# Kernel optimization log

Hardware: AMD Instinct MI355X
Metric: run time of the kernel (lower is better)

The kernel has to match this reference:

```python
import jax, jax.numpy as jnp
import numpy as np

EPS = 1e-5      # numerical floor for degrees / std / attenuation
LEAK = 0.01     # LeakyReLU slope of mixing FCLayer
AVG_D = 3.3     # log(avg_degree + 1) from init_kwargs
BIG = 1e30      # masking constant for max/min aggregators


def setup_inputs() -> dict:
    key = jax.random.key(0)
    ks = jax.random.split(key, 12)
    B, N, Din, De, H = 8, 256, 128, 64, 128
    s = 0.05
    inp = {
        "input": jax.random.normal(ks[0], (B, N, Din), jnp.float32),
        "adj": (jax.random.uniform(ks[1], (B, N, N)) < 0.1).astype(jnp.float32),
        "adj_features": jax.random.normal(ks[2], (B, N, N, De), jnp.float32),
        "hidden": jnp.zeros((B * N, H), jnp.float32),
        "pre_W": jax.random.normal(ks[3], (2 * Din + De, Din), jnp.float32) * s,
        "pre_b": jnp.zeros((Din,), jnp.float32),
        "post_W": jax.random.normal(ks[4], (13 * Din, H), jnp.float32) * s,
        "post_b": jnp.zeros((H,), jnp.float32),
        "mix_W": jax.random.normal(ks[5], (H, H), jnp.float32) * s,
        "mix_b": jnp.zeros((H,), jnp.float32),
        "gru_Wih": jax.random.normal(ks[6], (3 * H, H), jnp.float32) * s,
        "gru_Whh": jax.random.normal(ks[7], (3 * H, H), jnp.float32) * s,
    }
    return inp


def reference(input, adj, adj_features, hidden, pre_W, pre_b, post_W, post_b,
              mix_W, mix_b, gru_Wih, gru_Whh):
    B, N, Din = input.shape
    H = mix_W.shape[1]
    # --- pretrans MLP over all pairs: Linear([h_i, h_j, e_ij]) ---
    # split the weight into blocks so we never materialize h_cat (B,N,N,2Din+De)
    Wi, Wj, We = pre_W[:Din], pre_W[Din:2 * Din], pre_W[2 * Din:]
    hi = input @ Wi            # (B,N,Din)
    hj = input @ Wj            # (B,N,Din)
    h_mod = (hi[:, :, None, :] + hj[:, None, :, :]
             + jnp.einsum('bije,ek->bijk', adj_features, We) + pre_b)  # (B,N,N,Din)
    # --- multi-aggregator masked reduction over source axis j ---
    deg = jnp.sum(adj, axis=2)                       # (B,N)
    degc = jnp.maximum(deg, EPS)[..., None]          # (B,N,1)
    s1 = jnp.einsum('bij,bijk->bik', adj, h_mod)
    s2 = jnp.einsum('bij,bijk->bik', adj, h_mod * h_mod)
    mean = s1 / degc
    var = jnp.maximum(s2 / degc - mean * mean, 0.0)
    std = jnp.sqrt(var + EPS)
    mask = adj[..., None] > 0
    has_nb = (deg > 0)[..., None]
    mx = jnp.where(has_nb, jnp.max(jnp.where(mask, h_mod, -BIG), axis=2), 0.0)
    mn = jnp.where(has_nb, jnp.min(jnp.where(mask, h_mod, BIG), axis=2), 0.0)
    m = jnp.concatenate([mean, mx, mn, std], axis=2)  # (B,N,4*Din)
    # --- scalers: identity, amplification, attenuation ---
    slog = (jnp.log(deg + 1.0) / AVG_D)[..., None]    # (B,N,1)
    m = jnp.concatenate([m, m * slog, m / (slog + EPS)], axis=2)  # (B,N,12*Din)
    # --- posttrans Linear + mixing FCLayer (LeakyReLU) ---
    m_cat = jnp.concatenate([input, m], axis=2)       # (B,N,13*Din)
    y = m_cat @ post_W + post_b                       # (B,N,H)
    y = y @ mix_W + mix_b
    y = jnp.where(y > 0, y, LEAK * y)
    # --- GRUCell (bias=False), torch gate order r,z,n ---
    x = y.reshape(B * N, H)
    gi = x @ gru_Wih.T
    gh = hidden @ gru_Whh.T
    r = jax.nn.sigmoid(gi[:, :H] + gh[:, :H])
    z = jax.nn.sigmoid(gi[:, H:2 * H] + gh[:, H:2 * H])
    n = jnp.tanh(gi[:, 2 * H:] + r * gh[:, 2 * H:])
    h_new = (1.0 - z) * n + z * hidden
    return h_new.reshape(B, N, H)
```

## Files before the change

### kernel.cpp

```cpp
#include <hip/hip_runtime.h>
#include <cstdint>
#include <cstddef>

#define EPSF 1e-5f
#define LEAKF 0.01f
#define AVGD 3.3f

static constexpr int Nn = 256, DIN = 128, DE = 64, Hn = 128;
static constexpr int BN = 2048;
static constexpr int CT = 1664;

typedef short bf16x8 __attribute__((ext_vector_type(8)));
typedef float f32x4  __attribute__((ext_vector_type(4)));
union BF8 { bf16x8 v; uint16_t u[8]; };

__device__ __forceinline__ float bf2f(uint16_t u) { return __uint_as_float(((uint32_t)u) << 16); }
__device__ __forceinline__ float bflo(uint32_t u)  { return __uint_as_float(u << 16); }
__device__ __forceinline__ uint16_t f2bf(float f) {
  uint32_t u = __float_as_uint(f);
  u += 0x7fffu + ((u >> 16) & 1u);
  return (uint16_t)(u >> 16);
}

__device__ __forceinline__ int detect_bf16(const uint32_t* w) {
  float lo = bflo(w[threadIdx.x & 63]);
  unsigned long long ok = __ballot(fabsf(lo) < 64.f);
  return ok == 0xFFFFFFFFFFFFFFFFull;
}
__device__ __forceinline__ float loadf(const void* p, size_t i, int isbf) {
  return isbf ? bf2f(((const uint16_t*)p)[i]) : ((const float*)p)[i];
}
__device__ __forceinline__ f32x4 mfma16(bf16x8 a, bf16x8 b, f32x4 c) {
  return __builtin_amdgcn_mfma_f32_16x16x32_bf16(a, b, c, 0, 0, 0);
}

__global__ __launch_bounds__(256) void k_prep(
    const void* __restrict__ input, const void* __restrict__ pre_W,
    const void* __restrict__ post_W, const void* __restrict__ mix_W,
    const void* __restrict__ Wih, const void* __restrict__ Whh,
    const void* __restrict__ hidden,
    uint16_t* __restrict__ preWb, uint16_t* __restrict__ postTb,
    uint16_t* __restrict__ mixTb, uint16_t* __restrict__ Wihb,
    uint16_t* __restrict__ Whhb, uint16_t* __restrict__ hidb,
    uint16_t* __restrict__ Ab) {
  int isbf = detect_bf16((const uint32_t*)input);
  int b = blockIdx.x, tid = threadIdx.x;
  if (b < 232) {
    if (b >= 16 && b < 24) return;
    __shared__ float tile[32][33];
    const void* src; int off, R, C, t; uint16_t* bdst;
    if (b < 16)      { src = mix_W;  off = 0; bdst = mixTb;  R = 128;  C = 128; t = b; }
    else             { src = post_W; off = 0; bdst = postTb; R = 1664; C = 128; t = b - 24; }
    int bx = t & 3, by = t >> 2;
    int tx = tid & 31, ty = tid >> 5;
    int c0 = bx * 32, r0 = by * 32;
    #pragma unroll
    for (int dy = 0; dy < 32; dy += 8) {
      size_t idx = (size_t)off + (size_t)(r0 + ty + dy) * C + (c0 + tx);
      tile[ty + dy][tx] = loadf(src, idx, isbf);
    }
    __syncthreads();
    #pragma unroll
    for (int dy = 0; dy < 32; dy += 8)
      bdst[(size_t)(c0 + ty + dy) * R + (r0 + tx)] = f2bf(tile[tx][ty + dy]);
  } else if (b < 428 && b >= 300) {
    int idx = (b - 300) * 2048 + tid * 8;
    int node = idx >> 7, col = idx & 127;
    uint16_t v[8];
    if (isbf) *(uint4*)v = *(const uint4*)((const uint16_t*)input + idx);
    else { const float* s = (const float*)input + idx;
           #pragma unroll
           for (int e = 0; e < 8; e++) v[e] = f2bf(s[e]); }
    *(uint4*)(Ab + (size_t)node * CT + col) = *(uint4*)v;
  } else {
    const void* src; uint16_t* dst; int base;
    if (b < 252)      { src = pre_W;  dst = preWb; base = (b - 232) * 2048; }
    else if (b < 276) { src = Wih;    dst = Wihb;  base = (b - 252) * 2048; }
    else if (b < 300) { src = Whh;    dst = Whhb;  base = (b - 276) * 2048; }
    else              { src = hidden; dst = hidb;  base = (b - 428) * 2048; }
    int i = base + tid * 8;
    uint16_t v[8];
    if (isbf) *(uint4*)v = *(const uint4*)((const uint16_t*)src + i);
    else { const float* s = (const float*)src + i;
           #pragma unroll
           for (int e = 0; e < 8; e++) v[e] = f2bf(s[e]); }
    *(uint4*)(dst + i) = *(uint4*)v;
  }
}

__global__ __launch_bounds__(256) void k1_mfma(
    const uint16_t* __restrict__ Ab, const uint16_t* __restrict__ preWb,
    const void* __restrict__ pre_b, const void* __restrict__ input_flag,
    float* __restrict__ hi, float* __restrict__ hj) {
  int isbf = detect_bf16((const uint32_t*)input_flag);
  int tid = threadIdx.x;
  int lane = tid & 63, w = tid >> 6;
  int wg = blockIdx.x * 4 + w;
  int rt = wg >> 4, nt = wg & 15;
  int ishj = nt >> 3, ct = nt & 7;
  int m16 = lane & 15, quad = lane >> 4;
  int col = ct * 16 + m16;
  const uint16_t* ap = Ab + (size_t)(rt * 16 + m16) * CT + quad * 8;
  int kbase = ishj ? 128 : 0;
  f32x4 acc = {0.f, 0.f, 0.f, 0.f};
  #pragma unroll
  for (int kt = 0; kt < 4; kt++) {
    bf16x8 a = *(const bf16x8*)(ap + kt * 32);
    BF8 bb;
    #pragma unroll
    for (int j = 0; j < 8; j++)
      bb.u[j] = preWb[(size_t)(kbase + kt * 32 + quad * 8 + j) * 128 + col];
    acc = mfma16(a, bb.v, acc);
  }
  float bias = ishj ? 0.f : loadf(pre_b, col, isbf);
  float* dst = ishj ? hj : hi;
  #pragma unroll
  for (int r = 0; r < 4; r++)
    dst[(size_t)(rt * 16 + quad * 4 + r) * 128 + col] = acc[r] + bias;
}

__global__ __launch_bounds__(256) void k2_mfma(
    const void* __restrict__ input, const void* __restrict__ adj_raw,
    const void* __restrict__ af_raw,
    const float* __restrict__ hi, const float* __restrict__ hj,
    const uint16_t* __restrict__ preWb, uint16_t* __restrict__ Ab) {
  __shared__ int s_cnt;
  __shared__ int nbr[Nn];
  __shared__ __align__(16) uint16_t A_lds[16 * 72];
  int isbf = detect_bf16((const uint32_t*)input);
  int bi = blockIdx.x, tid = threadIdx.x;
  if (tid == 0) s_cnt = 0;
  __syncthreads();
  {
    float a = loadf(adj_raw, (size_t)bi * Nn + tid, isbf);
    if (a > 0.f) nbr[atomicAdd(&s_cnt, 1)] = tid;
  }
  __syncthreads();
  int cnt = s_cnt;

  int lane = tid & 63, w = tid >> 6;
  int m16 = lane & 15, quad = lane >> 4;
  int col0 = w * 32 + m16, col1 = col0 + 16;

  BF8 b00, b01, b10, b11;
  #pragma unroll
  for (int j = 0; j < 8; j++) {
    int k0 = 256 + quad * 8 + j, k1 = k0 + 32;
    b00.u[j] = preWb[(size_t)k0 * 128 + col0];
    b01.u[j] = preWb[(size_t)k1 * 128 + col0];
    b10.u[j] = preWb[(size_t)k0 * 128 + col1];
    b11.u[j] = preWb[(size_t)k1 * 128 + col1];
  }
  float base0 = hi[(size_t)bi * 128 + col0];
  float base1 = hi[(size_t)bi * 128 + col1];
  const float* hjb = &hj[(size_t)(bi & ~(Nn - 1)) * 128];

  float s1a = 0.f, s2a = 0.f, mxa = -1e30f, mna = 1e30f;
  float s1b = 0.f, s2b = 0.f, mxb = -1e30f, mnb = 1e30f;

  for (int ce = 0; ce < cnt; ce += 16) {
    __syncthreads();
    if (tid < 128) {
      int e = tid >> 3, seg = tid & 7;
      int ei = ce + e; if (ei >= cnt) ei = cnt - 1;
      int j = nbr[ei];
      uint16_t v[8];
      if (isbf)
        *(uint4*)v = *(const uint4*)((const uint16_t*)af_raw + ((size_t)bi * Nn + j) * DE + seg * 8);
      else {
        const float* s = (const float*)af_raw + ((size_t)bi * Nn + j) * DE + seg * 8;
        #pragma unroll
        for (int x = 0; x < 8; x++) v[x] = f2bf(s[x]);
      }
      *(uint4*)&A_lds[e * 72 + seg * 8] = *(uint4*)v;
    }
    __syncthreads();
    float hjv0[4], hjv1[4]; int vld[4];
    #pragma unroll
    for (int r = 0; r < 4; r++) {
      int e = ce + quad * 4 + r;
      vld[r] = (e < cnt);
      int j = nbr[vld[r] ? e : (cnt - 1)];
      hjv0[r] = hjb[(size_t)j * 128 + col0];
      hjv1[r] = hjb[(size_t)j * 128 + col1];
    }
    bf16x8 a0 = *(const bf16x8*)&A_lds[m16 * 72 + quad * 8];
    bf16x8 a1 = *(const bf16x8*)&A_lds[m16 * 72 + 32 + quad * 8];
    f32x4 C0 = {0.f,0.f,0.f,0.f}, C1 = C0;
    C0 = mfma16(a0, b00.v, C0); C0 = mfma16(a1, b01.v, C0);
    C1 = mfma16(a0, b10.v, C1); C1 = mfma16(a1, b11.v, C1);
    #pragma unroll
    for (int r = 0; r < 4; r++) {
      float h0 = base0 + hjv0[r] + C0[r];
      float h1 = base1 + hjv1[r] + C1[r];
      if (vld[r]) {
        s1a += h0; s2a += h0 * h0; mxa = fmaxf(mxa, h0); mna = fminf(mna, h0);
        s1b += h1; s2b += h1 * h1; mxb = fmaxf(mxb, h1); mnb = fminf(mnb, h1);
      }
    }
  }
  #pragma unroll
  for (int off = 16; off <= 32; off <<= 1) {
    s1a += __shfl_xor(s1a, off); s2a += __shfl_xor(s2a, off);
    mxa = fmaxf(mxa, __shfl_xor(mxa, off)); mna = fminf(mna, __shfl_xor(mna, off));
    s1b += __shfl_xor(s1b, off); s2b += __shfl_xor(s2b, off);
    mxb = fmaxf(mxb, __shfl_xor(mxb, off)); mnb = fminf(mnb, __shfl_xor(mnb, off));
  }
  if (quad == 0) {
    float deg = (float)cnt, degc = fmaxf(deg, EPSF);
    float slog = logf(deg + 1.f) / AVGD;
    float inv  = 1.f / (slog + EPSF);
    uint16_t* mo = Ab + (size_t)bi * CT + 128;
    #pragma unroll
    for (int t = 0; t < 2; t++) {
      float s1 = t ? s1b : s1a, s2 = t ? s2b : s2a;
      float mx = t ? mxb : mxa, mn = t ? mnb : mna;
      int col = t ? col1 : col0;
      float mean = s1 / degc;
      float var  = fmaxf(s2 / degc - mean * mean, 0.f);
      float stdv = sqrtf(var + EPSF);
      if (cnt == 0) { mx = 0.f; mn = 0.f; }
      mo[0*128+col]  = f2bf(mean);        mo[1*128+col]  = f2bf(mx);
      mo[2*128+col]  = f2bf(mn);          mo[3*128+col]  = f2bf(stdv);
      mo[4*128+col]  = f2bf(mean * slog); mo[5*128+col]  = f2bf(mx * slog);
      mo[6*128+col]  = f2bf(mn * slog);   mo[7*128+col]  = f2bf(stdv * slog);
      mo[8*128+col]  = f2bf(mean * inv);  mo[9*128+col]  = f2bf(mx * inv);
      mo[10*128+col] = f2bf(mn * inv);    mo[11*128+col] = f2bf(stdv * inv);
    }
  }
}

__global__ __launch_bounds__(256) void k3a(
    const uint16_t* __restrict__ Ab, const uint16_t* __restrict__ postTb,
    const void* __restrict__ post_b, const void* __restrict__ input_flag,
    uint16_t* __restrict__ yb) {
  int isbf = detect_bf16((const uint32_t*)input_flag);
  int tid = threadIdx.x;
  int lane = tid & 63, w = tid >> 6;
  int wg = blockIdx.x * 4 + w;
  int rt = wg >> 3, ct = wg & 7;
  int m16 = lane & 15, quad = lane >> 4;
  const uint16_t* ap = Ab     + (size_t)(rt * 16 + m16) * CT + quad * 8;
  const uint16_t* bp = postTb + (size_t)(ct * 16 + m16) * CT + quad * 8;
  f32x4 acc0 = {0.f,0.f,0.f,0.f}, acc1 = acc0;
  #pragma unroll 4
  for (int kt = 0; kt < 52; kt += 2) {
    bf16x8 a0 = *(const bf16x8*)(ap + kt * 32);
    bf16x8 b0 = *(const bf16x8*)(bp + kt * 32);
    bf16x8 a1 = *(const bf16x8*)(ap + kt * 32 + 32);
    bf16x8 b1 = *(const bf16x8*)(bp + kt * 32 + 32);
    acc0 = mfma16(a0, b0, acc0);
    acc1 = mfma16(a1, b1, acc1);
  }
  int col = ct * 16 + m16;
  float pb = loadf(post_b, col, isbf);
  #pragma unroll
  for (int r = 0; r < 4; r++)
    yb[(size_t)(rt * 16 + quad * 4 + r) * 128 + col] = f2bf(acc0[r] + acc1[r] + pb);
}

__global__ __launch_bounds__(512) void k3b(
    const uint16_t* __restrict__ yb, const uint16_t* __restrict__ mixTb,
    const void* __restrict__ mix_b, const uint16_t* __restrict__ Wihb,
    const uint16_t* __restrict__ Whhb, const uint16_t* __restrict__ hidb,
    const void* __restrict__ input_flag, void* __restrict__ out) {
  constexpr int SX = 136;
  __shared__ __align__(16) uint16_t x_s[16 * SX];
  __shared__ __align__(16) uint16_t hid_s[16 * SX];
  int isbf = detect_bf16((const uint32_t*)input_flag);
  int tid = threadIdx.x;
  int n0 = blockIdx.x * 16;
  if (tid < 256) {
    int row = tid >> 4, c = (tid & 15) * 8;
    *(uint4*)&hid_s[row * SX + c] = *(const uint4*)&hidb[(size_t)(n0 + row) * 128 + c];
  }
  int lane = tid & 63, w = tid >> 6;
  int m16 = lane & 15, quad = lane >> 4;
  int col = w * 16 + m16;

  f32x4 acc = {0.f,0.f,0.f,0.f};
  const uint16_t* ya = yb    + (size_t)(n0 + m16) * 128 + quad * 8;
  const uint16_t* mb = mixTb + (size_t)col * 128 + quad * 8;
  #pragma unroll
  for (int kt = 0; kt < 4; kt++)
    acc = mfma16(*(const bf16x8*)(ya + kt * 32), *(const bf16x8*)(mb + kt * 32), acc);
  float mbias = loadf(mix_b, col, isbf);
  __syncthreads();
  #pragma unroll
  for (int r = 0; r < 4; r++) {
    float v = acc[r] + mbias; v = v > 0.f ? v : LEAKF * v;
    x_s[(quad * 4 + r) * SX + col] = f2bf(v);
  }
  __syncthreads();

  f32x4 gi[3], gh[3];
  #pragma unroll
  for (int q = 0; q < 3; q++) { gi[q] = {0.f,0.f,0.f,0.f}; gh[q] = {0.f,0.f,0.f,0.f}; }
  const uint16_t* xa = &x_s[m16 * SX + quad * 8];
  const uint16_t* ha = &hid_s[m16 * SX + quad * 8];
  #pragma unroll
  for (int kt = 0; kt < 4; kt++) {
    bf16x8 ax = *(const bf16x8*)(xa + kt * 32);
    bf16x8 ah = *(const bf16x8*)(ha + kt * 32);
    #pragma unroll
    for (int q = 0; q < 3; q++) {
      bf16x8 bi = *(const bf16x8*)&Wihb[(size_t)(q * 128 + col) * 128 + kt * 32 + quad * 8];
      bf16x8 bh = *(const bf16x8*)&Whhb[(size_t)(q * 128 + col) * 128 + kt * 32 + quad * 8];
      gi[q] = mfma16(ax, bi, gi[q]);
      gh[q] = mfma16(ah, bh, gh[q]);
    }
  }
  #pragma unroll
  for (int r = 0; r < 4; r++) {
    int row = quad * 4 + r;
    float rg = 1.f / (1.f + expf(-(gi[0][r] + gh[0][r])));
    float zg = 1.f / (1.f + expf(-(gi[1][r] + gh[1][r])));
    float ng = tanhf(gi[2][r] + rg * gh[2][r]);
    float hv = bf2f(hid_s[row * SX + col]);
    float res = (1.f - zg) * ng + zg * hv;
    size_t oi = (size_t)(n0 + row) * 128 + col;
    if (isbf) ((uint16_t*)out)[oi] = f2bf(res);
    else      ((float*)out)[oi]    = res;
  }
}

extern "C" void kernel_launch(void* const* d_in, const int* in_sizes, int n_in,
                              void* d_out, int out_size, void* d_ws, size_t ws_size,
                              hipStream_t stream) {
  const void* input  = d_in[0];
  const void* adj    = d_in[1];
  const void* af     = d_in[2];
  const void* hidden = d_in[3];
  const void* pre_W  = d_in[4];
  const void* pre_b  = d_in[5];
  const void* post_W = d_in[6];
  const void* post_b = d_in[7];
  const void* mix_W  = d_in[8];
  const void* mix_b  = d_in[9];
  const void* Wih    = d_in[10];
  const void* Whh    = d_in[11];

  float* ws = (float*)d_ws;
  float* hi = ws;
  float* hj = hi + 262144;
  uint16_t* Ab     = (uint16_t*)(hj + 262144);
  uint16_t* postTb = Ab + (size_t)BN * CT;
  uint16_t* mixTb  = postTb + 212992;
  uint16_t* preWb  = mixTb + 16384;
  uint16_t* Wihb   = preWb + 40960;
  uint16_t* Whhb   = Wihb + 49152;
  uint16_t* hidb   = Whhb + 49152;
  uint16_t* yb     = hidb + 262144;

  k_prep<<<556, 256, 0, stream>>>(input, pre_W, post_W, mix_W, Wih, Whh, hidden,
                                  preWb, postTb, mixTb, Wihb, Whhb, hidb, Ab);
  k1_mfma<<<512, 256, 0, stream>>>(Ab, preWb, pre_b, input, hi, hj);
  k2_mfma<<<BN, 256, 0, stream>>>(input, adj, af, hi, hj, preWb, Ab);
  k3a<<<256, 256, 0, stream>>>(Ab, postTb, post_b, input, yb);
  k3b<<<128, 512, 0, stream>>>(yb, mixTb, mix_b, Wihb, Whhb, hidb, input, d_out);
}
```

Measured before the change: 227.5 us.

## Fuse hi/hj GEMM into prep, drop LDS staging in k2, split-K in k3a

The hi/hj projection is folded into the prep kernel, which now converts input and pre_W inline, so one kernel launch goes away. pre_W is stored transposed so k2 can load its B fragments with vector loads. k2 now builds its neighbor list with a wave ballot and prefix popcount instead of shared atomics, and loads edge features straight into MFMA registers, removing the per-chunk LDS staging and barriers. k3a splits K across wave pairs and reduces the halves through LDS, doubling the grid for more parallelism at the cost of an extra sync.

```diff
diff --git a/kernel.cpp b/kernel.cpp
--- a/kernel.cpp
+++ b/kernel.cpp
@@ -38,33 +38,45 @@
     const void* __restrict__ input, const void* __restrict__ pre_W,
     const void* __restrict__ post_W, const void* __restrict__ mix_W,
     const void* __restrict__ Wih, const void* __restrict__ Whh,
-    const void* __restrict__ hidden,
-    uint16_t* __restrict__ preWb, uint16_t* __restrict__ postTb,
+    const void* __restrict__ hidden, const void* __restrict__ pre_b,
+    uint16_t* __restrict__ preWTb, uint16_t* __restrict__ postTb,
     uint16_t* __restrict__ mixTb, uint16_t* __restrict__ Wihb,
     uint16_t* __restrict__ Whhb, uint16_t* __restrict__ hidb,
-    uint16_t* __restrict__ Ab) {
+    uint16_t* __restrict__ Ab, float* __restrict__ hi, float* __restrict__ hj) {
   int isbf = detect_bf16((const uint32_t*)input);
   int b = blockIdx.x, tid = threadIdx.x;
-  if (b < 232) {
-    if (b >= 16 && b < 24) return;
+  if (b < 264) {
     __shared__ float tile[32][33];
-    const void* src; int off, R, C, t; uint16_t* bdst;
-    if (b < 16)      { src = mix_W;  off = 0; bdst = mixTb;  R = 128;  C = 128; t = b; }
-    else             { src = post_W; off = 0; bdst = postTb; R = 1664; C = 128; t = b - 24; }
+    const void* src; int R, C, t; uint16_t* bdst;
+    if (b < 16)       { src = mix_W;  R = 128;  C = 128; t = b;       bdst = mixTb; }
+    else if (b < 224) { src = post_W; R = 1664; C = 128; t = b - 16;  bdst = postTb; }
+    else              { src = pre_W;  R = 320;  C = 128; t = b - 224; bdst = preWTb; }
     int bx = t & 3, by = t >> 2;
     int tx = tid & 31, ty = tid >> 5;
     int c0 = bx * 32, r0 = by * 32;
     #pragma unroll
     for (int dy = 0; dy < 32; dy += 8) {
-      size_t idx = (size_t)off + (size_t)(r0 + ty + dy) * C + (c0 + tx);
+      size_t idx = (size_t)(r0 + ty + dy) * C + (c0 + tx);
       tile[ty + dy][tx] = loadf(src, idx, isbf);
     }
     __syncthreads();
     #pragma unroll
     for (int dy = 0; dy < 32; dy += 8)
       bdst[(size_t)(c0 + ty + dy) * R + (r0 + tx)] = f2bf(tile[tx][ty + dy]);
-  } else if (b < 428 && b >= 300) {
-    int idx = (b - 300) * 2048 + tid * 8;
+  } else if (b < 440) {
+    const void* src; uint16_t* dst; int base;
+    if (b < 288)      { src = Wih;    dst = Wihb; base = (b - 264) * 2048; }
+    else if (b < 312) { src = Whh;    dst = Whhb; base = (b - 288) * 2048; }
+    else              { src = hidden; dst = hidb; base = (b - 312) * 2048; }
+    int i = base + tid * 8;
+    uint16_t v[8];
+    if (isbf) *(uint4*)v = *(const uint4*)((const uint16_t*)src + i);
+    else { const float* s = (const float*)src + i;
+           #pragma unroll
+           for (int e = 0; e < 8; e++) v[e] = f2bf(s[e]); }
+    *(uint4*)(dst + i) = *(uint4*)v;
+  } else if (b < 568) {
+    int idx = (b - 440) * 2048 + tid * 8;
     int node = idx >> 7, col = idx & 127;
     uint16_t v[8];
     if (isbf) *(uint4*)v = *(const uint4*)((const uint16_t*)input + idx);
@@ -73,84 +85,70 @@
            for (int e = 0; e < 8; e++) v[e] = f2bf(s[e]); }
     *(uint4*)(Ab + (size_t)node * CT + col) = *(uint4*)v;
   } else {
-    const void* src; uint16_t* dst; int base;
-    if (b < 252)      { src = pre_W;  dst = preWb; base = (b - 232) * 2048; }
-    else if (b < 276) { src = Wih;    dst = Wihb;  base = (b - 252) * 2048; }
-    else if (b < 300) { src = Whh;    dst = Whhb;  base = (b - 276) * 2048; }
-    else              { src = hidden; dst = hidb;  base = (b - 428) * 2048; }
-    int i = base + tid * 8;
-    uint16_t v[8];
-    if (isbf) *(uint4*)v = *(const uint4*)((const uint16_t*)src + i);
-    else { const float* s = (const float*)src + i;
-           #pragma unroll
-           for (int e = 0; e < 8; e++) v[e] = f2bf(s[e]); }
-    *(uint4*)(dst + i) = *(uint4*)v;
-  }
-}
-
-__global__ __launch_bounds__(256) void k1_mfma(
-    const uint16_t* __restrict__ Ab, const uint16_t* __restrict__ preWb,
-    const void* __restrict__ pre_b, const void* __restrict__ input_flag,
-    float* __restrict__ hi, float* __restrict__ hj) {
-  int isbf = detect_bf16((const uint32_t*)input_flag);
-  int tid = threadIdx.x;
-  int lane = tid & 63, w = tid >> 6;
-  int wg = blockIdx.x * 4 + w;
-  int rt = wg >> 4, nt = wg & 15;
-  int ishj = nt >> 3, ct = nt & 7;
-  int m16 = lane & 15, quad = lane >> 4;
-  int col = ct * 16 + m16;
-  const uint16_t* ap = Ab + (size_t)(rt * 16 + m16) * CT + quad * 8;
-  int kbase = ishj ? 128 : 0;
-  f32x4 acc = {0.f, 0.f, 0.f, 0.f};
-  #pragma unroll
-  for (int kt = 0; kt < 4; kt++) {
-    bf16x8 a = *(const bf16x8*)(ap + kt * 32);
-    BF8 bb;
-    #pragma unroll
-    for (int j = 0; j < 8; j++)
-      bb.u[j] = preWb[(size_t)(kbase + kt * 32 + quad * 8 + j) * 128 + col];
-    acc = mfma16(a, bb.v, acc);
-  }
-  float bias = ishj ? 0.f : loadf(pre_b, col, isbf);
-  float* dst = ishj ? hj : hi;
-  #pragma unroll
-  for (int r = 0; r < 4; r++)
-    dst[(size_t)(rt * 16 + quad * 4 + r) * 128 + col] = acc[r] + bias;
+    int lane = tid & 63, w = tid >> 6;
+    int wg = (b - 568) * 4 + w;
+    int rt = wg >> 4, nt = wg & 15;
+    int ishj = nt >> 3, ct = nt & 7;
+    int m16 = lane & 15, quad = lane >> 4;
+    int col = ct * 16 + m16;
+    int row = rt * 16 + m16;
+    int kbase = ishj ? 128 : 0;
+    f32x4 acc = {0.f, 0.f, 0.f, 0.f};
+    #pragma unroll
+    for (int kt = 0; kt < 4; kt++) {
+      bf16x8 av;
+      if (isbf) av = *(const bf16x8*)((const uint16_t*)input + (size_t)row * 128 + kt * 32 + quad * 8);
+      else { const float* s = (const float*)input + (size_t)row * 128 + kt * 32 + quad * 8;
+             BF8 t;
+             #pragma unroll
+             for (int e = 0; e < 8; e++) t.u[e] = f2bf(s[e]);
+             av = t.v; }
+      BF8 bb;
+      #pragma unroll
+      for (int j = 0; j < 8; j++) {
+        size_t wi = (size_t)(kbase + kt * 32 + quad * 8 + j) * 128 + col;
+        bb.u[j] = isbf ? ((const uint16_t*)pre_W)[wi] : f2bf(((const float*)pre_W)[wi]);
+      }
+      acc = mfma16(av, bb.v, acc);
+    }
+    float bias = ishj ? 0.f : loadf(pre_b, col, isbf);
+    float* dst = ishj ? hj : hi;
+    #pragma unroll
+    for (int r = 0; r < 4; r++)
+      dst[(size_t)(rt * 16 + quad * 4 + r) * 128 + col] = acc[r] + bias;
+  }
 }
 
 __global__ __launch_bounds__(256) void k2_mfma(
     const void* __restrict__ input, const void* __restrict__ adj_raw,
     const void* __restrict__ af_raw,
     const float* __restrict__ hi, const float* __restrict__ hj,
-    const uint16_t* __restrict__ preWb, uint16_t* __restrict__ Ab) {
-  __shared__ int s_cnt;
+    const uint16_t* __restrict__ preWTb, uint16_t* __restrict__ Ab) {
   __shared__ int nbr[Nn];
-  __shared__ __align__(16) uint16_t A_lds[16 * 72];
+  __shared__ int wcnt[4];
   int isbf = detect_bf16((const uint32_t*)input);
   int bi = blockIdx.x, tid = threadIdx.x;
-  if (tid == 0) s_cnt = 0;
-  __syncthreads();
-  {
-    float a = loadf(adj_raw, (size_t)bi * Nn + tid, isbf);
-    if (a > 0.f) nbr[atomicAdd(&s_cnt, 1)] = tid;
-  }
-  __syncthreads();
-  int cnt = s_cnt;
-
   int lane = tid & 63, w = tid >> 6;
+
+  float a = loadf(adj_raw, (size_t)bi * Nn + tid, isbf);
+  unsigned long long bm = __ballot(a > 0.f);
+  int pre = __popcll(bm & ((1ull << lane) - 1ull));
+  if (lane == 0) wcnt[w] = __popcll(bm);
+  __syncthreads();
+  int base = 0, cnt = 0;
+  #pragma unroll
+  for (int i = 0; i < 4; i++) { if (i < w) base += wcnt[i]; cnt += wcnt[i]; }
+  if (a > 0.f) nbr[base + pre] = tid;
+  __syncthreads();
+
   int m16 = lane & 15, quad = lane >> 4;
   int col0 = w * 32 + m16, col1 = col0 + 16;
 
-  BF8 b00, b01, b10, b11;
-  #pragma unroll
-  for (int j = 0; j < 8; j++) {
-    int k0 = 256 + quad * 8 + j, k1 = k0 + 32;
-    b00.u[j] = preWb[(size_t)k0 * 128 + col0];
-    b01.u[j] = preWb[(size_t)k1 * 128 + col0];
-    b10.u[j] = preWb[(size_t)k0 * 128 + col1];
-    b11.u[j] = preWb[(size_t)k1 * 128 + col1];
-  }
+  bf16x8 b00 = *(const bf16x8*)&preWTb[(size_t)col0 * 320 + 256 + quad * 8];
+  bf16x8 b01 = *(const bf16x8*)&preWTb[(size_t)col0 * 320 + 288 + quad * 8];
+  bf16x8 b10 = *(const bf16x8*)&preWTb[(size_t)col1 * 320 + 256 + quad * 8];
+  bf16x8 b11 = *(const bf16x8*)&preWTb[(size_t)col1 * 320 + 288 + quad * 8];
+
   float base0 = hi[(size_t)bi * 128 + col0];
   float base1 = hi[(size_t)bi * 128 + col1];
   const float* hjb = &hj[(size_t)(bi & ~(Nn - 1)) * 128];
@@ -159,36 +157,35 @@
   float s1b = 0.f, s2b = 0.f, mxb = -1e30f, mnb = 1e30f;
 
   for (int ce = 0; ce < cnt; ce += 16) {
-    __syncthreads();
-    if (tid < 128) {
-      int e = tid >> 3, seg = tid & 7;
-      int ei = ce + e; if (ei >= cnt) ei = cnt - 1;
-      int j = nbr[ei];
-      uint16_t v[8];
-      if (isbf)
-        *(uint4*)v = *(const uint4*)((const uint16_t*)af_raw + ((size_t)bi * Nn + j) * DE + seg * 8);
-      else {
-        const float* s = (const float*)af_raw + ((size_t)bi * Nn + j) * DE + seg * 8;
-        #pragma unroll
-        for (int x = 0; x < 8; x++) v[x] = f2bf(s[x]);
+    int ei = ce + m16; if (ei >= cnt) ei = cnt - 1;
+    int j = nbr[ei];
+    bf16x8 a0, a1;
+    if (isbf) {
+      const uint16_t* ar = (const uint16_t*)af_raw + ((size_t)bi * Nn + j) * DE;
+      a0 = *(const bf16x8*)(ar + quad * 8);
+      a1 = *(const bf16x8*)(ar + 32 + quad * 8);
+    } else {
+      const float* ar = (const float*)af_raw + ((size_t)bi * Nn + j) * DE;
+      BF8 t0, t1;
+      #pragma unroll
+      for (int e = 0; e < 8; e++) {
+        t0.u[e] = f2bf(ar[quad * 8 + e]);
+        t1.u[e] = f2bf(ar[32 + quad * 8 + e]);
       }
-      *(uint4*)&A_lds[e * 72 + seg * 8] = *(uint4*)v;
-    }
-    __syncthreads();
+      a0 = t0.v; a1 = t1.v;
+    }
     float hjv0[4], hjv1[4]; int vld[4];
     #pragma unroll
     for (int r = 0; r < 4; r++) {
       int e = ce + quad * 4 + r;
       vld[r] = (e < cnt);
-      int j = nbr[vld[r] ? e : (cnt - 1)];
-      hjv0[r] = hjb[(size_t)j * 128 + col0];
-      hjv1[r] = hjb[(size_t)j * 128 + col1];
-    }
-    bf16x8 a0 = *(const bf16x8*)&A_lds[m16 * 72 + quad * 8];
-    bf16x8 a1 = *(const bf16x8*)&A_lds[m16 * 72 + 32 + quad * 8];
+      int jj = nbr[vld[r] ? e : (cnt - 1)];
+      hjv0[r] = hjb[(size_t)jj * 128 + col0];
+      hjv1[r] = hjb[(size_t)jj * 128 + col1];
+    }
     f32x4 C0 = {0.f,0.f,0.f,0.f}, C1 = C0;
-    C0 = mfma16(a0, b00.v, C0); C0 = mfma16(a1, b01.v, C0);
-    C1 = mfma16(a0, b10.v, C1); C1 = mfma16(a1, b11.v, C1);
+    C0 = mfma16(a0, b00, C0); C0 = mfma16(a1, b01, C0);
+    C1 = mfma16(a0, b10, C1); C1 = mfma16(a1, b11, C1);
     #pragma unroll
     for (int r = 0; r < 4; r++) {
       float h0 = base0 + hjv0[r] + C0[r];
@@ -234,29 +231,35 @@
     const uint16_t* __restrict__ Ab, const uint16_t* __restrict__ postTb,
     const void* __restrict__ post_b, const void* __restrict__ input_flag,
     uint16_t* __restrict__ yb) {
+  __shared__ float red[2][16][17];
   int isbf = detect_bf16((const uint32_t*)input_flag);
   int tid = threadIdx.x;
   int lane = tid & 63, w = tid >> 6;
-  int wg = blockIdx.x * 4 + w;
-  int rt = wg >> 3, ct = wg & 7;
+  int wid = blockIdx.x * 4 + w;
+  int tile = wid >> 1, kh = wid & 1, pair = w >> 1;
+  int rt = tile >> 3, ct = tile & 7;
   int m16 = lane & 15, quad = lane >> 4;
-  const uint16_t* ap = Ab     + (size_t)(rt * 16 + m16) * CT + quad * 8;
-  const uint16_t* bp = postTb + (size_t)(ct * 16 + m16) * CT + quad * 8;
+  const uint16_t* ap = Ab     + (size_t)(rt * 16 + m16) * CT + kh * 832 + quad * 8;
+  const uint16_t* bp = postTb + (size_t)(ct * 16 + m16) * CT + kh * 832 + quad * 8;
   f32x4 acc0 = {0.f,0.f,0.f,0.f}, acc1 = acc0;
-  #pragma unroll 4
-  for (int kt = 0; kt < 52; kt += 2) {
-    bf16x8 a0 = *(const bf16x8*)(ap + kt * 32);
-    bf16x8 b0 = *(const bf16x8*)(bp + kt * 32);
-    bf16x8 a1 = *(const bf16x8*)(ap + kt * 32 + 32);
-    bf16x8 b1 = *(const bf16x8*)(bp + kt * 32 + 32);
-    acc0 = mfma16(a0, b0, acc0);
-    acc1 = mfma16(a1, b1, acc1);
-  }
-  int col = ct * 16 + m16;
-  float pb = loadf(post_b, col, isbf);
-  #pragma unroll
-  for (int r = 0; r < 4; r++)
-    yb[(size_t)(rt * 16 + quad * 4 + r) * 128 + col] = f2bf(acc0[r] + acc1[r] + pb);
+  #pragma unroll 13
+  for (int kt = 0; kt < 26; kt += 2) {
+    acc0 = mfma16(*(const bf16x8*)(ap + kt * 32),      *(const bf16x8*)(bp + kt * 32),      acc0);
+    acc1 = mfma16(*(const bf16x8*)(ap + kt * 32 + 32), *(const bf16x8*)(bp + kt * 32 + 32), acc1);
+  }
+  if (kh == 1) {
+    #pragma unroll
+    for (int r = 0; r < 4; r++) red[pair][quad * 4 + r][m16] = acc0[r] + acc1[r];
+  }
+  __syncthreads();
+  if (kh == 0) {
+    int col = ct * 16 + m16;
+    float pb = loadf(post_b, col, isbf);
+    #pragma unroll
+    for (int r = 0; r < 4; r++)
+      yb[(size_t)(rt * 16 + quad * 4 + r) * 128 + col] =
+          f2bf(acc0[r] + acc1[r] + red[pair][quad * 4 + r][m16] + pb);
+  }
 }
 
 __global__ __launch_bounds__(512) void k3b(
@@ -346,16 +349,15 @@
   uint16_t* Ab     = (uint16_t*)(hj + 262144);
   uint16_t* postTb = Ab + (size_t)BN * CT;
   uint16_t* mixTb  = postTb + 212992;
-  uint16_t* preWb  = mixTb + 16384;
-  uint16_t* Wihb   = preWb + 40960;
+  uint16_t* preWTb = mixTb + 16384;
+  uint16_t* Wihb   = preWTb + 40960;
   uint16_t* Whhb   = Wihb + 49152;
   uint16_t* hidb   = Whhb + 49152;
   uint16_t* yb     = hidb + 262144;
 
-  k_prep<<<556, 256, 0, stream>>>(input, pre_W, post_W, mix_W, Wih, Whh, hidden,
-                                  preWb, postTb, mixTb, Wihb, Whhb, hidb, Ab);
-  k1_mfma<<<512, 256, 0, stream>>>(Ab, preWb, pre_b, input, hi, hj);
-  k2_mfma<<<BN, 256, 0, stream>>>(input, adj, af, hi, hj, preWb, Ab);
-  k3a<<<256, 256, 0, stream>>>(Ab, postTb, post_b, input, yb);
+  k_prep<<<1080, 256, 0, stream>>>(input, pre_W, post_W, mix_W, Wih, Whh, hidden, pre_b,
+                                   preWTb, postTb, mixTb, Wihb, Whhb, hidb, Ab, hi, hj);
+  k2_mfma<<<BN, 256, 0, stream>>>(input, adj, af, hi, hj, preWTb, Ab);
+  k3a<<<512, 256, 0, stream>>>(Ab, postTb, post_b, input, yb);
   k3b<<<128, 512, 0, stream>>>(yb, mixTb, mix_b, Wihb, Whhb, hidb, input, d_out);
 }
```

After: 236.0 us. +3.7%, slower.
